# Kernel tuning notes

Hardware: AMD Instinct MI355X
Metric: run time of the kernel (lower is better)

Reference implementation:

```python
import jax, jax.numpy as jnp
import numpy as np

B, S, H, SSZ, IN = 1024, 100, 128, 100, 2


def _gru(x, h, Wih, Whh, bih, bhh):
    # PyTorch GRU cell: gates ordered (reset, update, new)
    gx = x @ Wih.T + bih
    gh = h @ Whh.T + bhh
    xr, xz, xn = jnp.split(gx, 3, axis=-1)
    hr, hz, hn = jnp.split(gh, 3, axis=-1)
    r = jax.nn.sigmoid(xr + hr)
    z = jax.nn.sigmoid(xz + hz)
    n = jnp.tanh(xn + r * hn)
    return (1.0 - z) * n + z * h


def _attn(inst_h, rnn_out, W, v):
    # inst_h: [B,S,H], rnn_out: [B,H] -> softmax attention weights [B,S]
    h = jnp.concatenate([inst_h, jnp.broadcast_to(rnn_out[:, None, :], inst_h.shape)], axis=-1)
    s = jax.nn.relu(jnp.einsum('bsk,kh->bsh', h, W)) @ v
    return jax.nn.softmax(s, axis=1)


def setup_inputs() -> dict:
    key = jax.random.key(0)
    k = jax.random.split(key, 32)
    p = lambda i, shape, sc=0.05: sc * jax.random.normal(k[i], shape, jnp.float32)
    instance = jax.random.uniform(k[0], (B, S, IN), jnp.float32)
    # solutions must be per-row permutations of node indices
    solution_1 = jnp.argsort(jax.random.uniform(k[1], (B, S)), axis=1).astype(jnp.int32)
    solution_2 = jnp.argsort(jax.random.uniform(k[2], (B, S)), axis=1).astype(jnp.int32)
    eps = jax.random.normal(k[3], (B, SSZ), jnp.float32)
    return dict(
        instance=instance, solution_1=solution_1, solution_2=solution_2, eps=eps,
        emb_i_W=p(4, (H, IN)), emb_i_b=jnp.zeros(H, jnp.float32),
        emb_r_W=p(5, (H, IN)), emb_r_b=jnp.zeros(H, jnp.float32),
        attn_W=p(6, (2 * H, H)), attn_v=p(7, (H,)),
        gru_Wih=p(8, (3 * H, H)), gru_Whh=p(9, (3 * H, H)),
        gru_bih=jnp.zeros(3 * H, jnp.float32), gru_bhh=jnp.zeros(3 * H, jnp.float32),
        grud_Wih=p(10, (3 * H, 2 * H)), grud_Whh=p(11, (3 * H, H)),
        grud_bih=jnp.zeros(3 * H, jnp.float32), grud_bhh=jnp.zeros(3 * H, jnp.float32),
        enc_fc1_W=p(12, (SSZ, H)), enc_fc1_b=jnp.zeros(SSZ, jnp.float32),
        enc_fc2_W=p(13, (SSZ, H)), enc_fc2_b=jnp.zeros(SSZ, jnp.float32),
        ptr_W=p(14, (2 * H, H)), ptr_v=p(15, (H,)),
        pfc1_W=p(16, (2 * H, 2 * H + SSZ)), pfc1_b=jnp.zeros(2 * H, jnp.float32),
        pfc2_W=p(17, (H, 2 * H)), pfc2_b=jnp.zeros(H, jnp.float32),
    )


def reference(instance, solution_1, solution_2, eps,
              emb_i_W, emb_i_b, emb_r_W, emb_r_b, attn_W, attn_v,
              gru_Wih, gru_Whh, gru_bih, gru_bhh,
              grud_Wih, grud_Whh, grud_bih, grud_bhh,
              enc_fc1_W, enc_fc1_b, enc_fc2_W, enc_fc2_b,
              ptr_W, ptr_v, pfc1_W, pfc1_b, pfc2_W, pfc2_b):
    b_idx = jnp.arange(B)
    inst_h = instance @ emb_i_W.T + emb_i_b  # [B,S,H]
    emb_r = lambda x: x @ emb_r_W.T + emb_r_b
    take = lambda ptr: instance[b_idx, ptr]  # gather node coords [B,IN]

    # ---------------- Encoder ----------------
    def enc_step(carry, ptr):
        h1, h2, ref_h = carry
        h1 = _gru(ref_h, h1, gru_Wih, gru_Whh, gru_bih, gru_bhh)
        a = _attn(inst_h, h1, attn_W, attn_v)
        context = jnp.einsum('bs,bsh->bh', a, inst_h)
        ref_h = emb_r(take(ptr))
        rnn_in = jnp.concatenate([ref_h, context], axis=-1)  # [B,2H]
        h2 = _gru(rnn_in, h2, grud_Wih, grud_Whh, grud_bih, grud_bhh)
        return (h1, h2, ref_h), None

    z0 = jnp.zeros((B, H), instance.dtype)
    ref_h0 = emb_r(take(solution_1[:, 0]))
    (_, h2, _), _ = jax.lax.scan(enc_step, (z0, z0, ref_h0), solution_1[:, 1:].T)
    mu = h2 @ enc_fc1_W.T + enc_fc1_b
    log_var = h2 @ enc_fc2_W.T + enc_fc2_b
    Z = mu + eps * jnp.exp(0.5 * log_var)

    # ---------------- Decoder (teacher forcing) ----------------
    mask0 = jnp.ones((B, S), instance.dtype).at[b_idx, solution_2[:, 0]].set(0.0)

    def dec_step(carry, ptr):
        h1, ref_in, mask = carry
        ref_h = emb_r(ref_in)
        h1 = _gru(ref_h, h1, gru_Wih, gru_Whh, gru_bih, gru_bhh)
        a = _attn(inst_h, h1, attn_W, attn_v)
        context = jnp.einsum('bs,bsh->bh', a, inst_h)
        fc_in = jnp.concatenate([context, Z, ref_h], axis=-1)  # [B, 2H+SSZ]
        fc_out = (fc_in @ pfc1_W.T + pfc1_b) @ pfc2_W.T + pfc2_b  # no activation, as in torch
        hcat = jnp.concatenate([inst_h, jnp.broadcast_to(fc_out[:, None, :], inst_h.shape)], axis=-1)
        logits = jnp.tanh(jnp.einsum('bsk,kh->bsh', hcat, ptr_W)) @ ptr_v  # [B,S]
        probs = jax.nn.softmax(logits + jnp.log(mask), axis=1)
        logp = jnp.log(probs[b_idx, ptr])
        pred = jnp.argmax(probs, axis=1)
        mask = mask.at[b_idx, ptr].set(0.0)  # tsp.update_mask: mark chosen node visited
        return (h1, take(ptr), mask), (pred, logp)

    init = (z0, take(solution_2[:, 0]), mask0)
    _, (preds, logps) = jax.lax.scan(dec_step, init, solution_2[:, 1:].T)
    tour_idx = jnp.concatenate([solution_2[:, :1], preds.T.astype(solution_2.dtype)], axis=1)
    tour_logp = logps.T  # [B, S-1]
    return (mu, log_var, Z, tour_idx, tour_logp)
```

## Files before the change

### kernel.cpp

```cpp
#include <hip/hip_runtime.h>
#include <math.h>

static constexpr int NB  = 1024;
static constexpr int NS  = 100;
static constexpr int NH  = 128;
static constexpr int GPB = 2;
static constexpr int NTHR = 256;
static constexpr int NBLK = NB / GPB;

static constexpr int OUT_MU = 0;
static constexpr int OUT_LV = NB * NS;
static constexpr int OUT_Z  = 2 * NB * NS;
static constexpr int OUT_TI = 3 * NB * NS;
static constexpr int OUT_LP = 4 * NB * NS;

#define NEGF (-3.4e38f)

template<int C4>
__device__ __forceinline__ void dot2x3f(const float* __restrict__ wr0,
        const float* __restrict__ wr1, const float* __restrict__ wr2,
        const float* __restrict__ x0, const float* __restrict__ x1,
        float& r00, float& r01, float& r10, float& r11, float& r20, float& r21)
{
    const float4* W0 = reinterpret_cast<const float4*>(wr0);
    const float4* W1 = reinterpret_cast<const float4*>(wr1);
    const float4* W2 = reinterpret_cast<const float4*>(wr2);
    const float4* X0 = reinterpret_cast<const float4*>(x0);
    const float4* X1 = reinterpret_cast<const float4*>(x1);
    float a00 = 0.f, a01 = 0.f, a10 = 0.f, a11 = 0.f, a20 = 0.f, a21 = 0.f;
    #pragma unroll 8
    for (int c = 0; c < C4; ++c) {
        float4 u0 = W0[c], u1 = W1[c], u2 = W2[c];
        float4 v0 = X0[c], v1 = X1[c];
        a00 = fmaf(u0.x, v0.x, a00); a00 = fmaf(u0.y, v0.y, a00); a00 = fmaf(u0.z, v0.z, a00); a00 = fmaf(u0.w, v0.w, a00);
        a01 = fmaf(u0.x, v1.x, a01); a01 = fmaf(u0.y, v1.y, a01); a01 = fmaf(u0.z, v1.z, a01); a01 = fmaf(u0.w, v1.w, a01);
        a10 = fmaf(u1.x, v0.x, a10); a10 = fmaf(u1.y, v0.y, a10); a10 = fmaf(u1.z, v0.z, a10); a10 = fmaf(u1.w, v0.w, a10);
        a11 = fmaf(u1.x, v1.x, a11); a11 = fmaf(u1.y, v1.y, a11); a11 = fmaf(u1.z, v1.z, a11); a11 = fmaf(u1.w, v1.w, a11);
        a20 = fmaf(u2.x, v0.x, a20); a20 = fmaf(u2.y, v0.y, a20); a20 = fmaf(u2.z, v0.z, a20); a20 = fmaf(u2.w, v0.w, a20);
        a21 = fmaf(u2.x, v1.x, a21); a21 = fmaf(u2.y, v1.y, a21); a21 = fmaf(u2.z, v1.z, a21); a21 = fmaf(u2.w, v1.w, a21);
    }
    r00 = a00; r01 = a01; r10 = a10; r11 = a11; r20 = a20; r21 = a21;
}

template<int C4>
__device__ __forceinline__ void dot2f(const float* __restrict__ w,
        const float* __restrict__ x0, const float* __restrict__ x1, float& r0, float& r1)
{
    const float4* W = reinterpret_cast<const float4*>(w);
    const float4* X0 = reinterpret_cast<const float4*>(x0);
    const float4* X1 = reinterpret_cast<const float4*>(x1);
    float a0 = 0.f, a1 = 0.f;
    #pragma unroll 8
    for (int c = 0; c < C4; ++c) {
        float4 u = W[c];
        float4 v0 = X0[c], v1 = X1[c];
        a0 = fmaf(u.x, v0.x, a0); a0 = fmaf(u.y, v0.y, a0); a0 = fmaf(u.z, v0.z, a0); a0 = fmaf(u.w, v0.w, a0);
        a1 = fmaf(u.x, v1.x, a1); a1 = fmaf(u.y, v1.y, a1); a1 = fmaf(u.z, v1.z, a1); a1 = fmaf(u.w, v1.w, a1);
    }
    r0 = a0; r1 = a1;
}

template<int C4>
__device__ __forceinline__ void dot1f(const float* __restrict__ w,
        const float* __restrict__ x0, float& r0)
{
    const float4* W = reinterpret_cast<const float4*>(w);
    const float4* X0 = reinterpret_cast<const float4*>(x0);
    float a0 = 0.f;
    #pragma unroll 8
    for (int c = 0; c < C4; ++c) {
        float4 u = W[c];
        float4 v0 = X0[c];
        a0 = fmaf(u.x, v0.x, a0); a0 = fmaf(u.y, v0.y, a0); a0 = fmaf(u.z, v0.z, a0); a0 = fmaf(u.w, v0.w, a0);
    }
    r0 = a0;
}

template<int C4>
__device__ __forceinline__ double dotwd(const float* __restrict__ w, const float* __restrict__ x)
{
    const float4* W = reinterpret_cast<const float4*>(w);
    double a = 0.0;
    #pragma unroll 8
    for (int c = 0; c < C4; ++c) {
        float4 u = W[c];
        const float* p = x + 4 * c;
        a = fma((double)u.x, (double)p[0], a);
        a = fma((double)u.y, (double)p[1], a);
        a = fma((double)u.z, (double)p[2], a);
        a = fma((double)u.w, (double)p[3], a);
    }
    return a;
}

__device__ __forceinline__ void gruc(const float* __restrict__ bih, const float* __restrict__ bhh,
        const float* __restrict__ pa, const float* __restrict__ pb, float* __restrict__ h, int j)
{
    double r = 1.0 / (1.0 + exp(-(((double)pa[j]        + (double)bih[j])        + ((double)pb[j]        + (double)bhh[j]))));
    double z = 1.0 / (1.0 + exp(-(((double)pa[NH + j]   + (double)bih[NH + j])   + ((double)pb[NH + j]   + (double)bhh[NH + j]))));
    double n = tanh(((double)pa[2*NH + j] + (double)bih[2*NH + j]) + r * ((double)pb[2*NH + j] + (double)bhh[2*NH + j]));
    h[j] = (float)((1.0 - z) * n + z * (double)h[j]);
}

__global__ __launch_bounds__(NTHR) void vae_v14(
    const float* __restrict__ instance, const int* __restrict__ sol1,
    const int* __restrict__ sol2, const float* __restrict__ eps,
    const float* __restrict__ emb_i_W, const float* __restrict__ emb_i_b,
    const float* __restrict__ emb_r_W, const float* __restrict__ emb_r_b,
    const float* __restrict__ attn_W, const float* __restrict__ attn_v,
    const float* __restrict__ gru_Wih, const float* __restrict__ gru_Whh,
    const float* __restrict__ gru_bih, const float* __restrict__ gru_bhh,
    const float* __restrict__ grud_Wih, const float* __restrict__ grud_Whh,
    const float* __restrict__ grud_bih, const float* __restrict__ grud_bhh,
    const float* __restrict__ efc1_W, const float* __restrict__ efc1_b,
    const float* __restrict__ efc2_W, const float* __restrict__ efc2_b,
    const float* __restrict__ ptr_W, const float* __restrict__ ptr_v,
    const float* __restrict__ pfc1_W, const float* __restrict__ pfc1_b,
    const float* __restrict__ pfc2_W, const float* __restrict__ pfc2_b,
    float* __restrict__ out)
{
    __shared__ float  s_x[GPB][360];
    __shared__ float  s_h1[GPB][NH], s_h2[GPB][NH], s_fco[GPB][NH];
    __shared__ float  s_fch[GPB][256];
    __shared__ float  s_pa[GPB][3 * NH], s_pb[GPB][3 * NH];
    __shared__ double s_qh[GPB][NH];
    __shared__ double s_qpA[GPB][NH], s_qpB[GPB][NH];
    __shared__ double2 dAa[NH], dAp[NH];
    __shared__ double dAba[NH], dAbp[NH];
    __shared__ float  s_lg[GPB][NS], s_a[GPB][NS];
    __shared__ float  s_c0[GPB][NS], s_c1[GPB][NS], s_msk[GPB][NS];
    __shared__ float  t_wi0[NH], t_wi1[NH], t_bi[NH];
    __shared__ float  t_wr0[NH], t_wr1[NH], t_br[NH];
    __shared__ float  t_va[NH], t_vp[NH];
    __shared__ float  t_gbih[3*NH], t_gbhh[3*NH], t_dbih[3*NH], t_dbhh[3*NH];
    __shared__ float  t_p1b[256], t_p2b[NH];
    __shared__ int    s_sol1[GPB][NS], s_sol2[GPB][NS];
    __shared__ float  s_red[GPB][2];
    __shared__ double s_redd[GPB][2];
    __shared__ int    s_ri[GPB][2];
    __shared__ float  s_rc0[GPB], s_rc1[GPB];

    const int tid = threadIdx.x;
    const int bbase = blockIdx.x * GPB;
    const int j = tid & (NH - 1);
    const int half = tid >> 7;
    const int g = half;
    const int lane = tid & 63;
    const int wid = (tid >> 6) & 1;

    if (tid < NH) {
        t_wi0[tid] = emb_i_W[2*tid]; t_wi1[tid] = emb_i_W[2*tid+1]; t_bi[tid] = emb_i_b[tid];
        t_wr0[tid] = emb_r_W[2*tid]; t_wr1[tid] = emb_r_W[2*tid+1]; t_br[tid] = emb_r_b[tid];
        t_va[tid] = attn_v[tid]; t_vp[tid] = ptr_v[tid];
        t_p2b[tid] = pfc2_b[tid];
    }
    t_p1b[tid] = pfc1_b[tid];
    for (int i = tid; i < 3 * NH; i += NTHR) {
        t_gbih[i] = gru_bih[i]; t_gbhh[i] = gru_bhh[i];
        t_dbih[i] = grud_bih[i]; t_dbhh[i] = grud_bhh[i];
    }
    for (int i = tid; i < GPB * NS; i += NTHR) {
        int gg = i / NS, s = i - gg * NS;
        s_c0[gg][s] = instance[(size_t)((bbase + gg) * NS + s) * 2 + 0];
        s_c1[gg][s] = instance[(size_t)((bbase + gg) * NS + s) * 2 + 1];
        s_sol1[gg][s] = sol1[(bbase + gg) * NS + s];
        s_sol2[gg][s] = sol2[(bbase + gg) * NS + s];
    }
    s_h1[g][j] = 0.f;
    s_h2[g][j] = 0.f;
    __syncthreads();
    {
        const float* Wm = (half == 0) ? attn_W : ptr_W;
        double a0 = 0.0, a1 = 0.0, ab = 0.0;
        for (int k = 0; k < NH; ++k) {
            double wv = (double)Wm[(size_t)k * NH + j];
            a0 = fma((double)t_wi0[k], wv, a0);
            a1 = fma((double)t_wi1[k], wv, a1);
            ab = fma((double)t_bi[k],  wv, ab);
        }
        if (half == 0) { dAa[j].x = a0; dAa[j].y = a1; dAba[j] = ab; }
        else           { dAp[j].x = a0; dAp[j].y = a1; dAbp[j] = ab; }
    }
    {
        int sp = s_sol1[g][0];
        s_x[g][j] = fmaf(s_c0[g][sp], t_wr0[j], fmaf(s_c1[g][sp], t_wr1[j], t_br[j]));
    }
    __syncthreads();

    for (int t = 1; t < NS; ++t) {
        if (half == 0) {
            float a00,a01,a10,a11,a20,a21;
            dot2x3f<32>(gru_Wih + (size_t)j * NH, gru_Wih + (size_t)(NH + j) * NH,
                        gru_Wih + (size_t)(2*NH + j) * NH, s_x[0], s_x[1],
                        a00,a01,a10,a11,a20,a21);
            s_pa[0][j] = a00;        s_pa[1][j] = a01;
            s_pa[0][NH + j] = a10;   s_pa[1][NH + j] = a11;
            s_pa[0][2*NH + j] = a20; s_pa[1][2*NH + j] = a21;
        } else {
            float a00,a01,a10,a11,a20,a21;
            dot2x3f<32>(gru_Whh + (size_t)j * NH, gru_Whh + (size_t)(NH + j) * NH,
                        gru_Whh + (size_t)(2*NH + j) * NH, s_h1[0], s_h1[1],
                        a00,a01,a10,a11,a20,a21);
            s_pb[0][j] = a00;        s_pb[1][j] = a01;
            s_pb[0][NH + j] = a10;   s_pb[1][NH + j] = a11;
            s_pb[0][2*NH + j] = a20; s_pb[1][2*NH + j] = a21;
        }
        __syncthreads();
        gruc(t_gbih, t_gbhh, s_pa[g], s_pb[g], s_h1[g], j);
        __syncthreads();
        {
            const float* col = attn_W + (size_t)NH * NH + j;
            const int k0 = half * 64;
            double a00=0.0,a01=0.0,a02=0.0,a03=0.0;
            double a10=0.0,a11=0.0,a12=0.0,a13=0.0;
            #pragma unroll 8
            for (int k = 0; k < 64; k += 4) {
                float w0 = col[(size_t)(k0+k+0) * NH];
                float w1 = col[(size_t)(k0+k+1) * NH];
                float w2 = col[(size_t)(k0+k+2) * NH];
                float w3 = col[(size_t)(k0+k+3) * NH];
                float4 h0 = *reinterpret_cast<const float4*>(&s_h1[0][k0+k]);
                float4 h1v = *reinterpret_cast<const float4*>(&s_h1[1][k0+k]);
                a00 = fma((double)w0, (double)h0.x, a00);
                a01 = fma((double)w1, (double)h0.y, a01);
                a02 = fma((double)w2, (double)h0.z, a02);
                a03 = fma((double)w3, (double)h0.w, a03);
                a10 = fma((double)w0, (double)h1v.x, a10);
                a11 = fma((double)w1, (double)h1v.y, a11);
                a12 = fma((double)w2, (double)h1v.z, a12);
                a13 = fma((double)w3, (double)h1v.w, a13);
            }
// ... 43 lines not shown
        }
        __syncthreads();
        {
            float w0 = t_wi0[j], w1 = t_wi1[j], bb = t_bi[j];
            double a0 = 0.0, a1 = 0.0, a2 = 0.0, a3 = 0.0;
            #pragma unroll 5
            for (int s = 0; s < NS; s += 4) {
                float ih0 = fmaf(s_c0[g][s+0], w0, fmaf(s_c1[g][s+0], w1, bb));
                float ih1 = fmaf(s_c0[g][s+1], w0, fmaf(s_c1[g][s+1], w1, bb));
                float ih2 = fmaf(s_c0[g][s+2], w0, fmaf(s_c1[g][s+2], w1, bb));
                float ih3 = fmaf(s_c0[g][s+3], w0, fmaf(s_c1[g][s+3], w1, bb));
                a0 += (double)s_a[g][s+0] * (double)ih0;
                a1 += (double)s_a[g][s+1] * (double)ih1;
                a2 += (double)s_a[g][s+2] * (double)ih2;
                a3 += (double)s_a[g][s+3] * (double)ih3;
            }
            s_x[g][NH + j] = (float)(((a0 + a1) + (a2 + a3)));
            int sp = s_sol1[g][t];
            s_x[g][j] = fmaf(s_c0[g][sp], t_wr0[j], fmaf(s_c1[g][sp], t_wr1[j], t_br[j]));
        }
        __syncthreads();
        if (half == 0) {
            float a00,a01,a10,a11,a20,a21;
            dot2x3f<64>(grud_Wih + (size_t)j * 256, grud_Wih + (size_t)(NH + j) * 256,
                        grud_Wih + (size_t)(2*NH + j) * 256, s_x[0], s_x[1],
                        a00,a01,a10,a11,a20,a21);
            s_pa[0][j] = a00;        s_pa[1][j] = a01;
            s_pa[0][NH + j] = a10;   s_pa[1][NH + j] = a11;
            s_pa[0][2*NH + j] = a20; s_pa[1][2*NH + j] = a21;
        } else {
            float a00,a01,a10,a11,a20,a21;
            dot2x3f<32>(grud_Whh + (size_t)j * NH, grud_Whh + (size_t)(NH + j) * NH,
                        grud_Whh + (size_t)(2*NH + j) * NH, s_h2[0], s_h2[1],
                        a00,a01,a10,a11,a20,a21);
            s_pb[0][j] = a00;        s_pb[1][j] = a01;
            s_pb[0][NH + j] = a10;   s_pb[1][NH + j] = a11;
            s_pb[0][2*NH + j] = a20; s_pb[1][2*NH + j] = a21;
        }
        __syncthreads();
        gruc(t_dbih, t_dbhh, s_pa[g], s_pb[g], s_h2[g], j);
        __syncthreads();
    }

    for (int idx = tid; idx < GPB * NS; idx += NTHR) {
        int gg = idx / NS, s = idx - gg * NS, b = bbase + gg;
        double mu = dotwd<32>(efc1_W + (size_t)s * NH, s_h2[gg]) + (double)efc1_b[s];
        double lv = dotwd<32>(efc2_W + (size_t)s * NH, s_h2[gg]) + (double)efc2_b[s];
        double z  = mu + (double)eps[(size_t)b * NS + s] * exp(0.5 * lv);
        out[OUT_MU + b * NS + s] = (float)mu;
        out[OUT_LV + b * NS + s] = (float)lv;
        out[OUT_Z  + b * NS + s] = (float)z;
        s_x[gg][NH + s] = (float)z;
    }
    for (int i = tid; i < GPB * NS; i += NTHR) {
        int gg = i / NS, s = i - gg * NS;
        s_msk[gg][s] = 1.f;
    }
    s_h1[g][j] = 0.f;
    __syncthreads();
    if (tid < GPB) {
        int b = bbase + tid;
        int s0 = s_sol2[tid][0];
        s_msk[tid][s0] = 0.f;
        s_rc0[tid] = s_c0[tid][s0];
        s_rc1[tid] = s_c1[tid][s0];
        out[OUT_TI + b * NS + 0] = (float)s0;
    }
    __syncthreads();

    for (int t = 1; t < NS; ++t) {
        s_x[g][228 + j] = fmaf(s_rc0[g], t_wr0[j], fmaf(s_rc1[g], t_wr1[j], t_br[j]));
        __syncthreads();
        if (half == 0) {
            float a00,a01,a10,a11,a20,a21;
            dot2x3f<32>(gru_Wih + (size_t)j * NH, gru_Wih + (size_t)(NH + j) * NH,
                        gru_Wih + (size_t)(2*NH + j) * NH, s_x[0]+228, s_x[1]+228,
                        a00,a01,a10,a11,a20,a21);
            s_pa[0][j] = a00;        s_pa[1][j] = a01;
            s_pa[0][NH + j] = a10;   s_pa[1][NH + j] = a11;
            s_pa[0][2*NH + j] = a20; s_pa[1][2*NH + j] = a21;
        } else {
            float a00,a01,a10,a11,a20,a21;
            dot2x3f<32>(gru_Whh + (size_t)j * NH, gru_Whh + (size_t)(NH + j) * NH,
                        gru_Whh + (size_t)(2*NH + j) * NH, s_h1[0], s_h1[1],
                        a00,a01,a10,a11,a20,a21);
            s_pb[0][j] = a00;        s_pb[1][j] = a01;
            s_pb[0][NH + j] = a10;   s_pb[1][NH + j] = a11;
            s_pb[0][2*NH + j] = a20; s_pb[1][2*NH + j] = a21;
        }
        __syncthreads();
        gruc(t_gbih, t_gbhh, s_pa[g], s_pb[g], s_h1[g], j);
        __syncthreads();
        {
            const float* col = attn_W + (size_t)NH * NH + j;
            const int k0 = half * 64;
            double a00=0.0,a01=0.0,a02=0.0,a03=0.0;
            double a10=0.0,a11=0.0,a12=0.0,a13=0.0;
            #pragma unroll 8
            for (int k = 0; k < 64; k += 4) {
                float w0 = col[(size_t)(k0+k+0) * NH];
                float w1 = col[(size_t)(k0+k+1) * NH];
                float w2 = col[(size_t)(k0+k+2) * NH];
                float w3 = col[(size_t)(k0+k+3) * NH];
                float4 h0 = *reinterpret_cast<const float4*>(&s_h1[0][k0+k]);
                float4 h1v = *reinterpret_cast<const float4*>(&s_h1[1][k0+k]);
                a00 = fma((double)w0, (double)h0.x, a00);
                a01 = fma((double)w1, (double)h0.y, a01);
                a02 = fma((double)w2, (double)h0.z, a02);
                a03 = fma((double)w3, (double)h0.w, a03);
                a10 = fma((double)w0, (double)h1v.x, a10);
                a11 = fma((double)w1, (double)h1v.y, a11);
                a12 = fma((double)w2, (double)h1v.z, a12);
                a13 = fma((double)w3, (double)h1v.w, a13);
            }
            if (half == 0) { s_qpA[0][j] = (a00+a01)+(a02+a03); s_qpA[1][j] = (a10+a11)+(a12+a13); }
            else           { s_qpB[0][j] = (a00+a01)+(a02+a03); s_qpB[1][j] = (a10+a11)+(a12+a13); }
        }
        __syncthreads();
        s_qh[g][j] = dAba[j] + (s_qpA[g][j] + s_qpB[g][j]);
        __syncthreads();
        if (j < NS) {
            double c00 = (double)s_c0[g][j], c10 = (double)s_c1[g][j];
            double acc0 = 0.0, acc1 = 0.0, acc2 = 0.0, acc3 = 0.0;
            #pragma unroll 4
            for (int h = 0; h < NH; h += 4) {
                double2 A0 = dAa[h+0], A1 = dAa[h+1], A2 = dAa[h+2], A3 = dAa[h+3];
                double p0 = fma(c00, A0.x, fma(c10, A0.y, s_qh[g][h+0]));
                double p1 = fma(c00, A1.x, fma(c10, A1.y, s_qh[g][h+1]));
                double p2 = fma(c00, A2.x, fma(c10, A2.y, s_qh[g][h+2]));
                double p3 = fma(c00, A3.x, fma(c10, A3.y, s_qh[g][h+3]));
                acc0 = fma(fmax(p0, 0.0), (double)t_va[h+0], acc0);
                acc1 = fma(fmax(p1, 0.0), (double)t_va[h+1], acc1);
                acc2 = fma(fmax(p2, 0.0), (double)t_va[h+2], acc2);
                acc3 = fma(fmax(p3, 0.0), (double)t_va[h+3], acc3);
            }
            s_lg[g][j] = (float)(((acc0 + acc1) + (acc2 + acc3)));
        }
        __syncthreads();
        {
            float a = s_lg[g][lane];
            float b = (lane + 64 < NS) ? s_lg[g][lane + 64] : NEGF;
            float m = fmaxf(a, b);
            m = fmaxf(m, __shfl_xor(m, 32)); m = fmaxf(m, __shfl_xor(m, 16));
            m = fmaxf(m, __shfl_xor(m, 8));  m = fmaxf(m, __shfl_xor(m, 4));
            m = fmaxf(m, __shfl_xor(m, 2));  m = fmaxf(m, __shfl_xor(m, 1));
            float fv = 0.f;
            if (j < NS) { fv = (float)exp((double)s_lg[g][j] - (double)m); s_a[g][j] = fv; }
            double ps = (double)fv;
            ps += __shfl_xor(ps, 32); ps += __shfl_xor(ps, 16);
            ps += __shfl_xor(ps, 8);  ps += __shfl_xor(ps, 4);
            ps += __shfl_xor(ps, 2);  ps += __shfl_xor(ps, 1);
            if (lane == 0) s_redd[g][wid] = ps;
        }
        __syncthreads();
        if (j < NS) {
            double se = s_redd[g][0] + s_redd[g][1];
            s_a[g][j] = (float)((double)s_a[g][j] / se);
        }
        __syncthreads();
        {
            float w0 = t_wi0[j], w1 = t_wi1[j], bb = t_bi[j];
            double a0 = 0.0, a1 = 0.0, a2 = 0.0, a3 = 0.0;
            #pragma unroll 5
            for (int s = 0; s < NS; s += 4) {
                float ih0 = fmaf(s_c0[g][s+0], w0, fmaf(s_c1[g][s+0], w1, bb));
                float ih1 = fmaf(s_c0[g][s+1], w0, fmaf(s_c1[g][s+1], w1, bb));
                float ih2 = fmaf(s_c0[g][s+2], w0, fmaf(s_c1[g][s+2], w1, bb));
                float ih3 = fmaf(s_c0[g][s+3], w0, fmaf(s_c1[g][s+3], w1, bb));
                a0 += (double)s_a[g][s+0] * (double)ih0;
                a1 += (double)s_a[g][s+1] * (double)ih1;
                a2 += (double)s_a[g][s+2] * (double)ih2;
                a3 += (double)s_a[g][s+3] * (double)ih3;
            }
            s_x[g][j] = (float)(((a0 + a1) + (a2 + a3)));
        }
        __syncthreads();
        {
            float r0, r1;
            dot2f<89>(pfc1_W + (size_t)tid * 356, s_x[0], s_x[1], r0, r1);
            float bb = t_p1b[tid];
            s_fch[0][tid] = r0 + bb; s_fch[1][tid] = r1 + bb;
        }
        __syncthreads();
        {
            float r0;
            dot1f<64>(pfc2_W + (size_t)j * 256, s_fch[g], r0);
            s_fco[g][j] = r0 + t_p2b[j];
        }
        __syncthreads();
        {
            const float* col = ptr_W + (size_t)NH * NH + j;
            const int k0 = half * 64;
            double a00=0.0,a01=0.0,a02=0.0,a03=0.0;
            double a10=0.0,a11=0.0,a12=0.0,a13=0.0;
            #pragma unroll 8
            for (int k = 0; k < 64; k += 4) {
                float w0 = col[(size_t)(k0+k+0) * NH];
                float w1 = col[(size_t)(k0+k+1) * NH];
                float w2 = col[(size_t)(k0+k+2) * NH];
                float w3 = col[(size_t)(k0+k+3) * NH];
                float4 f0 = *reinterpret_cast<const float4*>(&s_fco[0][k0+k]);
                float4 f1 = *reinterpret_cast<const float4*>(&s_fco[1][k0+k]);
                a00 = fma((double)w0, (double)f0.x, a00);
                a01 = fma((double)w1, (double)f0.y, a01);
                a02 = fma((double)w2, (double)f0.z, a02);
                a03 = fma((double)w3, (double)f0.w, a03);
                a10 = fma((double)w0, (double)f1.x, a10);
                a11 = fma((double)w1, (double)f1.y, a11);
                a12 = fma((double)w2, (double)f1.z, a12);
                a13 = fma((double)w3, (double)f1.w, a13);
            }
            if (half == 0) { s_qpA[0][j] = (a00+a01)+(a02+a03); s_qpA[1][j] = (a10+a11)+(a12+a13); }
            else           { s_qpB[0][j] = (a00+a01)+(a02+a03); s_qpB[1][j] = (a10+a11)+(a12+a13); }
        }
        __syncthreads();
        s_qh[g][j] = dAbp[j] + (s_qpA[g][j] + s_qpB[g][j]);
        __syncthreads();
        if (j < NS) {
            double c00 = (double)s_c0[g][j], c10 = (double)s_c1[g][j];
            double acc0 = 0.0, acc1 = 0.0, acc2 = 0.0, acc3 = 0.0;
            #pragma unroll 4
            for (int h = 0; h < NH; h += 4) {
                double2 A0 = dAp[h+0], A1 = dAp[h+1], A2 = dAp[h+2], A3 = dAp[h+3];
                double p0 = fma(c00, A0.x, fma(c10, A0.y, s_qh[g][h+0]));
                double p1 = fma(c00, A1.x, fma(c10, A1.y, s_qh[g][h+1]));
                double p2 = fma(c00, A2.x, fma(c10, A2.y, s_qh[g][h+2]));
                double p3 = fma(c00, A3.x, fma(c10, A3.y, s_qh[g][h+3]));
                acc0 = fma((double)tanhf((float)p0), (double)t_vp[h+0], acc0);
                acc1 = fma((double)tanhf((float)p1), (double)t_vp[h+1], acc1);
                acc2 = fma((double)tanhf((float)p2), (double)t_vp[h+2], acc2);
                acc3 = fma((double)tanhf((float)p3), (double)t_vp[h+3], acc3);
            }
            s_lg[g][j] = (float)(((acc0 + acc1) + (acc2 + acc3)));
        }
        __syncthreads();
        {
            float la = s_lg[g][lane];
            float ma = (s_msk[g][lane] > 0.f) ? la : NEGF;
            float lb = NEGF;
            if (lane + 64 < NS) lb = (s_msk[g][lane + 64] > 0.f) ? s_lg[g][lane + 64] : NEGF;
            float m = fmaxf(ma, lb);
            m = fmaxf(m, __shfl_xor(m, 32)); m = fmaxf(m, __shfl_xor(m, 16));
            m = fmaxf(m, __shfl_xor(m, 8));  m = fmaxf(m, __shfl_xor(m, 4));
            m = fmaxf(m, __shfl_xor(m, 2));  m = fmaxf(m, __shfl_xor(m, 1));
            float fv = 0.f;
            if (j < NS) {
                fv = (s_msk[g][j] > 0.f) ? (float)exp((double)s_lg[g][j] - (double)m) : 0.f;
                s_a[g][j] = fv;
            }
            float  bv = (j < NS) ? fv : -1.f;
            int    bi = (j < NS) ? j  : NS;
            double ps = (j < NS) ? (double)fv : 0.0;
            #pragma unroll
            for (int o = 32; o >= 1; o >>= 1) {
                float  ov = __shfl_xor(bv, o);
                int    oi = __shfl_xor(bi, o);
                double op = __shfl_xor(ps, o);
                ps += op;
                if (ov > bv || (ov == bv && oi < bi)) { bv = ov; bi = oi; }
            }
            if (lane == 0) { s_red[g][wid] = bv; s_ri[g][wid] = bi; s_redd[g][wid] = ps; }
        }
        __syncthreads();
        if (tid < GPB) {
            int gg = tid, b = bbase + gg;
            float m = -1.f; int mi = NS; double se = 0.0;
            for (int i = 0; i < 2; ++i) {
                se += s_redd[gg][i];
                float v = s_red[gg][i]; int vi = s_ri[gg][i];
                if (v > m || (v == m && vi < mi)) { m = v; mi = vi; }
            }
            int pt = s_sol2[gg][t];
            double logp = log((double)s_a[gg][pt] / se);
            out[OUT_TI + b * NS + t]             = (float)mi;
            out[OUT_LP + b * (NS - 1) + (t - 1)] = (float)logp;
            s_msk[gg][pt] = 0.f;
            s_rc0[gg] = s_c0[gg][pt];
            s_rc1[gg] = s_c1[gg][pt];
        }
        __syncthreads();
    }
}

extern "C" void kernel_launch(void* const* d_in, const int* in_sizes, int n_in,
                              void* d_out, int out_size, void* d_ws, size_t ws_size,
                              hipStream_t stream)
{
    (void)in_sizes; (void)n_in; (void)out_size; (void)d_ws; (void)ws_size;
    vae_v14<<<NBLK, NTHR, 0, stream>>>(
        (const float*)d_in[0], (const int*)d_in[1], (const int*)d_in[2], (const float*)d_in[3],
        (const float*)d_in[4], (const float*)d_in[5], (const float*)d_in[6], (const float*)d_in[7],
        (const float*)d_in[8], (const float*)d_in[9], (const float*)d_in[10], (const float*)d_in[11],
        (const float*)d_in[12], (const float*)d_in[13], (const float*)d_in[14], (const float*)d_in[15],
        (const float*)d_in[16], (const float*)d_in[17], (const float*)d_in[18], (const float*)d_in[19],
        (const float*)d_in[20], (const float*)d_in[21], (const float*)d_in[22], (const float*)d_in[23],
        (const float*)d_in[24], (const float*)d_in[25], (const float*)d_in[26], (const float*)d_in[27],
        (float*)d_out);
}
```

Measured before the change: 12.26 ms.

## Decouple GRU recurrence from per-step attention/pointer work, processing chunks of steps per wave

```diff
diff --git a/kernel.cpp b/kernel.cpp
--- a/kernel.cpp
+++ b/kernel.cpp
@@ -43,40 +43,6 @@
 }
 
 template<int C4>
-__device__ __forceinline__ void dot2f(const float* __restrict__ w,
-        const float* __restrict__ x0, const float* __restrict__ x1, float& r0, float& r1)
-{
-    const float4* W = reinterpret_cast<const float4*>(w);
-    const float4* X0 = reinterpret_cast<const float4*>(x0);
-    const float4* X1 = reinterpret_cast<const float4*>(x1);
-    float a0 = 0.f, a1 = 0.f;
-    #pragma unroll 8
-    for (int c = 0; c < C4; ++c) {
-        float4 u = W[c];
-        float4 v0 = X0[c], v1 = X1[c];
-        a0 = fmaf(u.x, v0.x, a0); a0 = fmaf(u.y, v0.y, a0); a0 = fmaf(u.z, v0.z, a0); a0 = fmaf(u.w, v0.w, a0);
-        a1 = fmaf(u.x, v1.x, a1); a1 = fmaf(u.y, v1.y, a1); a1 = fmaf(u.z, v1.z, a1); a1 = fmaf(u.w, v1.w, a1);
-    }
-    r0 = a0; r1 = a1;
-}
-
-template<int C4>
-__device__ __forceinline__ void dot1f(const float* __restrict__ w,
-        const float* __restrict__ x0, float& r0)
-{
-    const float4* W = reinterpret_cast<const float4*>(w);
-    const float4* X0 = reinterpret_cast<const float4*>(x0);
-    float a0 = 0.f;
-    #pragma unroll 8
-    for (int c = 0; c < C4; ++c) {
-        float4 u = W[c];
-        float4 v0 = X0[c];
-        a0 = fmaf(u.x, v0.x, a0); a0 = fmaf(u.y, v0.y, a0); a0 = fmaf(u.z, v0.z, a0); a0 = fmaf(u.w, v0.w, a0);
-    }
-    r0 = a0;
-}
-
-template<int C4>
 __device__ __forceinline__ double dotwd(const float* __restrict__ w, const float* __restrict__ x)
 {
     const float4* W = reinterpret_cast<const float4*>(w);
@@ -102,7 +68,7 @@
     h[j] = (float)((1.0 - z) * n + z * (double)h[j]);
 }
 
-__global__ __launch_bounds__(NTHR) void vae_v14(
+__global__ __launch_bounds__(NTHR) void vae_v15(
     const float* __restrict__ instance, const int* __restrict__ sol1,
     const int* __restrict__ sol2, const float* __restrict__ eps,
     const float* __restrict__ emb_i_W, const float* __restrict__ emb_i_b,
@@ -120,25 +86,33 @@
     float* __restrict__ out)
 {
     __shared__ float  s_x[GPB][360];
-    __shared__ float  s_h1[GPB][NH], s_h2[GPB][NH], s_fco[GPB][NH];
-    __shared__ float  s_fch[GPB][256];
+    __shared__ float  s_h1[GPB][NH], s_h2[GPB][NH];
     __shared__ float  s_pa[GPB][3 * NH], s_pb[GPB][3 * NH];
     __shared__ double s_qh[GPB][NH];
     __shared__ double s_qpA[GPB][NH], s_qpB[GPB][NH];
     __shared__ double2 dAa[NH], dAp[NH];
     __shared__ double dAba[NH], dAbp[NH];
     __shared__ float  s_lg[GPB][NS], s_a[GPB][NS];
-    __shared__ float  s_c0[GPB][NS], s_c1[GPB][NS], s_msk[GPB][NS];
+    __shared__ float  s_c0[GPB][NS], s_c1[GPB][NS];
     __shared__ float  t_wi0[NH], t_wi1[NH], t_bi[NH];
     __shared__ float  t_wr0[NH], t_wr1[NH], t_br[NH];
     __shared__ float  t_va[NH], t_vp[NH];
     __shared__ float  t_gbih[3*NH], t_gbhh[3*NH], t_dbih[3*NH], t_dbhh[3*NH];
     __shared__ float  t_p1b[256], t_p2b[NH];
     __shared__ int    s_sol1[GPB][NS], s_sol2[GPB][NS];
-    __shared__ float  s_red[GPB][2];
     __shared__ double s_redd[GPB][2];
-    __shared__ int    s_ri[GPB][2];
     __shared__ float  s_rc0[GPB], s_rc1[GPB];
+    __shared__ float    s_ref[GPB][NH];
+    __shared__ float    h1buf[8][GPB][NH];
+    __shared__ float    rcb0[GPB][9], rcb1[GPB][9];
+    __shared__ unsigned maskb[8][GPB][4];
+    __shared__ unsigned m_run[GPB][4];
+    __shared__ double   w_qh[4][NH];
+    __shared__ float    w_lg[4][NS];
+    __shared__ float    w_av[4][NS];
+    __shared__ float    w_x[4][360];
+    __shared__ float    w_fh[4][256];
+    __shared__ float    w_fo[4][NH];
 
     const int tid = threadIdx.x;
     const int bbase = blockIdx.x * GPB;
@@ -147,6 +121,7 @@
     const int g = half;
     const int lane = tid & 63;
     const int wid = (tid >> 6) & 1;
+    const int wv = tid >> 6;
 
     if (tid < NH) {
         t_wi0[tid] = emb_i_W[2*tid]; t_wi1[tid] = emb_i_W[2*tid+1]; t_bi[tid] = emb_i_b[tid];
@@ -173,10 +148,10 @@
         const float* Wm = (half == 0) ? attn_W : ptr_W;
         double a0 = 0.0, a1 = 0.0, ab = 0.0;
         for (int k = 0; k < NH; ++k) {
-            double wv = (double)Wm[(size_t)k * NH + j];
-            a0 = fma((double)t_wi0[k], wv, a0);
-            a1 = fma((double)t_wi1[k], wv, a1);
-            ab = fma((double)t_bi[k],  wv, ab);
+            double wv2 = (double)Wm[(size_t)k * NH + j];
+            a0 = fma((double)t_wi0[k], wv2, a0);
+            a1 = fma((double)t_wi1[k], wv2, a1);
+            ab = fma((double)t_bi[k],  wv2, ab);
         }
         if (half == 0) { dAa[j].x = a0; dAa[j].y = a1; dAba[j] = ab; }
         else           { dAp[j].x = a0; dAp[j].y = a1; dAbp[j] = ab; }
@@ -326,231 +301,257 @@
         out[OUT_Z  + b * NS + s] = (float)z;
         s_x[gg][NH + s] = (float)z;
     }
-    for (int i = tid; i < GPB * NS; i += NTHR) {
-        int gg = i / NS, s = i - gg * NS;
-        s_msk[gg][s] = 1.f;
-    }
     s_h1[g][j] = 0.f;
     __syncthreads();
     if (tid < GPB) {
         int b = bbase + tid;
         int s0 = s_sol2[tid][0];
-        s_msk[tid][s0] = 0.f;
+        m_run[tid][0] = 0xFFFFFFFFu; m_run[tid][1] = 0xFFFFFFFFu;
+        m_run[tid][2] = 0xFFFFFFFFu; m_run[tid][3] = 0xFu;
+        m_run[tid][s0 >> 5] &= ~(1u << (s0 & 31));
         s_rc0[tid] = s_c0[tid][s0];
         s_rc1[tid] = s_c1[tid][s0];
         out[OUT_TI + b * NS + 0] = (float)s0;
     }
     __syncthreads();
-
-    for (int t = 1; t < NS; ++t) {
-        s_x[g][228 + j] = fmaf(s_rc0[g], t_wr0[j], fmaf(s_rc1[g], t_wr1[j], t_br[j]));
-        __syncthreads();
-        if (half == 0) {
-            float a00,a01,a10,a11,a20,a21;
-            dot2x3f<32>(gru_Wih + (size_t)j * NH, gru_Wih + (size_t)(NH + j) * NH,
-                        gru_Wih + (size_t)(2*NH + j) * NH, s_x[0]+228, s_x[1]+228,
-                        a00,a01,a10,a11,a20,a21);
-            s_pa[0][j] = a00;        s_pa[1][j] = a01;
-            s_pa[0][NH + j] = a10;   s_pa[1][NH + j] = a11;
-            s_pa[0][2*NH + j] = a20; s_pa[1][2*NH + j] = a21;
-        } else {
-            float a00,a01,a10,a11,a20,a21;
-            dot2x3f<32>(gru_Whh + (size_t)j * NH, gru_Whh + (size_t)(NH + j) * NH,
-                        gru_Whh + (size_t)(2*NH + j) * NH, s_h1[0], s_h1[1],
-                        a00,a01,a10,a11,a20,a21);
-            s_pb[0][j] = a00;        s_pb[1][j] = a01;
-            s_pb[0][NH + j] = a10;   s_pb[1][NH + j] = a11;
-            s_pb[0][2*NH + j] = a20; s_pb[1][2*NH + j] = a21;
-        }
-        __syncthreads();
-        gruc(t_gbih, t_gbhh, s_pa[g], s_pb[g], s_h1[g], j);
-        __syncthreads();
-        {
-            const float* col = attn_W + (size_t)NH * NH + j;
-            const int k0 = half * 64;
-            double a00=0.0,a01=0.0,a02=0.0,a03=0.0;
-            double a10=0.0,a11=0.0,a12=0.0,a13=0.0;
-            #pragma unroll 8
-            for (int k = 0; k < 64; k += 4) {
-                float w0 = col[(size_t)(k0+k+0) * NH];
-                float w1 = col[(size_t)(k0+k+1) * NH];
-                float w2 = col[(size_t)(k0+k+2) * NH];
-                float w3 = col[(size_t)(k0+k+3) * NH];
-                float4 h0 = *reinterpret_cast<const float4*>(&s_h1[0][k0+k]);
-                float4 h1v = *reinterpret_cast<const float4*>(&s_h1[1][k0+k]);
-                a00 = fma((double)w0, (double)h0.x, a00);
-                a01 = fma((double)w1, (double)h0.y, a01);
-                a02 = fma((double)w2, (double)h0.z, a02);
-                a03 = fma((double)w3, (double)h0.w, a03);
-                a10 = fma((double)w0, (double)h1v.x, a10);
-                a11 = fma((double)w1, (double)h1v.y, a11);
-                a12 = fma((double)w2, (double)h1v.z, a12);
-                a13 = fma((double)w3, (double)h1v.w, a13);
-            }
-            if (half == 0) { s_qpA[0][j] = (a00+a01)+(a02+a03); s_qpA[1][j] = (a10+a11)+(a12+a13); }
-            else           { s_qpB[0][j] = (a00+a01)+(a02+a03); s_qpB[1][j] = (a10+a11)+(a12+a13); }
-        }
-        __syncthreads();
-        s_qh[g][j] = dAba[j] + (s_qpA[g][j] + s_qpB[g][j]);
-        __syncthreads();
-        if (j < NS) {
-            double c00 = (double)s_c0[g][j], c10 = (double)s_c1[g][j];
-            double acc0 = 0.0, acc1 = 0.0, acc2 = 0.0, acc3 = 0.0;
-            #pragma unroll 4
-            for (int h = 0; h < NH; h += 4) {
-                double2 A0 = dAa[h+0], A1 = dAa[h+1], A2 = dAa[h+2], A3 = dAa[h+3];
-                double p0 = fma(c00, A0.x, fma(c10, A0.y, s_qh[g][h+0]));
-                double p1 = fma(c00, A1.x, fma(c10, A1.y, s_qh[g][h+1]));
-                double p2 = fma(c00, A2.x, fma(c10, A2.y, s_qh[g][h+2]));
-                double p3 = fma(c00, A3.x, fma(c10, A3.y, s_qh[g][h+3]));
-                acc0 = fma(fmax(p0, 0.0), (double)t_va[h+0], acc0);
-                acc1 = fma(fmax(p1, 0.0), (double)t_va[h+1], acc1);
-                acc2 = fma(fmax(p2, 0.0), (double)t_va[h+2], acc2);
-                acc3 = fma(fmax(p3, 0.0), (double)t_va[h+3], acc3);
-            }
-            s_lg[g][j] = (float)(((acc0 + acc1) + (acc2 + acc3)));
-        }
-        __syncthreads();
-        {
-            float a = s_lg[g][lane];
-            float b = (lane + 64 < NS) ? s_lg[g][lane + 64] : NEGF;
-            float m = fmaxf(a, b);
-            m = fmaxf(m, __shfl_xor(m, 32)); m = fmaxf(m, __shfl_xor(m, 16));
-            m = fmaxf(m, __shfl_xor(m, 8));  m = fmaxf(m, __shfl_xor(m, 4));
-            m = fmaxf(m, __shfl_xor(m, 2));  m = fmaxf(m, __shfl_xor(m, 1));
-            float fv = 0.f;
-            if (j < NS) { fv = (float)exp((double)s_lg[g][j] - (double)m); s_a[g][j] = fv; }
-            double ps = (double)fv;
-            ps += __shfl_xor(ps, 32); ps += __shfl_xor(ps, 16);
-            ps += __shfl_xor(ps, 8);  ps += __shfl_xor(ps, 4);
-            ps += __shfl_xor(ps, 2);  ps += __shfl_xor(ps, 1);
-            if (lane == 0) s_redd[g][wid] = ps;
-        }
-        __syncthreads();
-        if (j < NS) {
-            double se = s_redd[g][0] + s_redd[g][1];
-            s_a[g][j] = (float)((double)s_a[g][j] / se);
-        }
-        __syncthreads();
-        {
-            float w0 = t_wi0[j], w1 = t_wi1[j], bb = t_bi[j];
-            double a0 = 0.0, a1 = 0.0, a2 = 0.0, a3 = 0.0;
-            #pragma unroll 5
-            for (int s = 0; s < NS; s += 4) {
-                float ih0 = fmaf(s_c0[g][s+0], w0, fmaf(s_c1[g][s+0], w1, bb));
-                float ih1 = fmaf(s_c0[g][s+1], w0, fmaf(s_c1[g][s+1], w1, bb));
-                float ih2 = fmaf(s_c0[g][s+2], w0, fmaf(s_c1[g][s+2], w1, bb));
-                float ih3 = fmaf(s_c0[g][s+3], w0, fmaf(s_c1[g][s+3], w1, bb));
-                a0 += (double)s_a[g][s+0] * (double)ih0;
-                a1 += (double)s_a[g][s+1] * (double)ih1;
-                a2 += (double)s_a[g][s+2] * (double)ih2;
-                a3 += (double)s_a[g][s+3] * (double)ih3;
-            }
-            s_x[g][j] = (float)(((a0 + a1) + (a2 + a3)));
-        }
-        __syncthreads();
-        {
-            float r0, r1;
-            dot2f<89>(pfc1_W + (size_t)tid * 356, s_x[0], s_x[1], r0, r1);
-            float bb = t_p1b[tid];
-            s_fch[0][tid] = r0 + bb; s_fch[1][tid] = r1 + bb;
-        }
-        __syncthreads();
-        {
-            float r0;
-            dot1f<64>(pfc2_W + (size_t)j * 256, s_fch[g], r0);
-            s_fco[g][j] = r0 + t_p2b[j];
-        }
-        __syncthreads();
-        {
-            const float* col = ptr_W + (size_t)NH * NH + j;
-            const int k0 = half * 64;
-            double a00=0.0,a01=0.0,a02=0.0,a03=0.0;
-            double a10=0.0,a11=0.0,a12=0.0,a13=0.0;
-            #pragma unroll 8
-            for (int k = 0; k < 64; k += 4) {
-                float w0 = col[(size_t)(k0+k+0) * NH];
-                float w1 = col[(size_t)(k0+k+1) * NH];
-                float w2 = col[(size_t)(k0+k+2) * NH];
-                float w3 = col[(size_t)(k0+k+3) * NH];
-                float4 f0 = *reinterpret_cast<const float4*>(&s_fco[0][k0+k]);
-                float4 f1 = *reinterpret_cast<const float4*>(&s_fco[1][k0+k]);
-                a00 = fma((double)w0, (double)f0.x, a00);
-                a01 = fma((double)w1, (double)f0.y, a01);
-                a02 = fma((double)w2, (double)f0.z, a02);
-                a03 = fma((double)w3, (double)f0.w, a03);
-                a10 = fma((double)w0, (double)f1.x, a10);
-                a11 = fma((double)w1, (double)f1.y, a11);
-                a12 = fma((double)w2, (double)f1.z, a12);
-                a13 = fma((double)w3, (double)f1.w, a13);
-            }
-            if (half == 0) { s_qpA[0][j] = (a00+a01)+(a02+a03); s_qpA[1][j] = (a10+a11)+(a12+a13); }
-            else           { s_qpB[0][j] = (a00+a01)+(a02+a03); s_qpB[1][j] = (a10+a11)+(a12+a13); }
-        }
-        __syncthreads();
-        s_qh[g][j] = dAbp[j] + (s_qpA[g][j] + s_qpB[g][j]);
-        __syncthreads();
-        if (j < NS) {
-            double c00 = (double)s_c0[g][j], c10 = (double)s_c1[g][j];
-            double acc0 = 0.0, acc1 = 0.0, acc2 = 0.0, acc3 = 0.0;
-            #pragma unroll 4
-            for (int h = 0; h < NH; h += 4) {
-                double2 A0 = dAp[h+0], A1 = dAp[h+1], A2 = dAp[h+2], A3 = dAp[h+3];
-                double p0 = fma(c00, A0.x, fma(c10, A0.y, s_qh[g][h+0]));
-                double p1 = fma(c00, A1.x, fma(c10, A1.y, s_qh[g][h+1]));
-                double p2 = fma(c00, A2.x, fma(c10, A2.y, s_qh[g][h+2]));
-                double p3 = fma(c00, A3.x, fma(c10, A3.y, s_qh[g][h+3]));
-                acc0 = fma((double)tanhf((float)p0), (double)t_vp[h+0], acc0);
-                acc1 = fma((double)tanhf((float)p1), (double)t_vp[h+1], acc1);
-                acc2 = fma((double)tanhf((float)p2), (double)t_vp[h+2], acc2);
-                acc3 = fma((double)tanhf((float)p3), (double)t_vp[h+3], acc3);
-            }
-            s_lg[g][j] = (float)(((acc0 + acc1) + (acc2 + acc3)));
-        }
-        __syncthreads();
-        {
-            float la = s_lg[g][lane];
-            float ma = (s_msk[g][lane] > 0.f) ? la : NEGF;
-            float lb = NEGF;
-            if (lane + 64 < NS) lb = (s_msk[g][lane + 64] > 0.f) ? s_lg[g][lane + 64] : NEGF;
-            float m = fmaxf(ma, lb);
-            m = fmaxf(m, __shfl_xor(m, 32)); m = fmaxf(m, __shfl_xor(m, 16));
-            m = fmaxf(m, __shfl_xor(m, 8));  m = fmaxf(m, __shfl_xor(m, 4));
-            m = fmaxf(m, __shfl_xor(m, 2));  m = fmaxf(m, __shfl_xor(m, 1));
-            float fv = 0.f;
-            if (j < NS) {
-                fv = (s_msk[g][j] > 0.f) ? (float)exp((double)s_lg[g][j] - (double)m) : 0.f;
-                s_a[g][j] = fv;
-            }
-            float  bv = (j < NS) ? fv : -1.f;
-            int    bi = (j < NS) ? j  : NS;
-            double ps = (j < NS) ? (double)fv : 0.0;
-            #pragma unroll
-            for (int o = 32; o >= 1; o >>= 1) {
-                float  ov = __shfl_xor(bv, o);
-                int    oi = __shfl_xor(bi, o);
-                double op = __shfl_xor(ps, o);
-                ps += op;
-                if (ov > bv || (ov == bv && oi < bi)) { bv = ov; bi = oi; }
-            }
-            if (lane == 0) { s_red[g][wid] = bv; s_ri[g][wid] = bi; s_redd[g][wid] = ps; }
-        }
-        __syncthreads();
+    s_ref[g][j] = fmaf(s_rc0[g], t_wr0[j], fmaf(s_rc1[g], t_wr1[j], t_br[j]));
+    __syncthreads();
+
+    for (int c = 0; c < 13; ++c) {
+        const int t0 = 1 + c * 8;
+        const int CHc = (t0 + 8 <= NS) ? 8 : (NS - t0);
         if (tid < GPB) {
-            int gg = tid, b = bbase + gg;
-            float m = -1.f; int mi = NS; double se = 0.0;
-            for (int i = 0; i < 2; ++i) {
-                se += s_redd[gg][i];
-                float v = s_red[gg][i]; int vi = s_ri[gg][i];
-                if (v > m || (v == m && vi < mi)) { m = v; mi = vi; }
-            }
-            int pt = s_sol2[gg][t];
-            double logp = log((double)s_a[gg][pt] / se);
-            out[OUT_TI + b * NS + t]             = (float)mi;
-            out[OUT_LP + b * (NS - 1) + (t - 1)] = (float)logp;
-            s_msk[gg][pt] = 0.f;
-            s_rc0[gg] = s_c0[gg][pt];
-            s_rc1[gg] = s_c1[gg][pt];
+            const int gg = tid;
+            for (int qi = 0; qi <= CHc; ++qi) {
+                int tt = t0 + qi;
+                if (qi < CHc) {
+                    maskb[qi][gg][0] = m_run[gg][0];
+                    maskb[qi][gg][1] = m_run[gg][1];
+                    maskb[qi][gg][2] = m_run[gg][2];
+                    maskb[qi][gg][3] = m_run[gg][3];
+                    int pt = s_sol2[gg][tt];
+                    m_run[gg][pt >> 5] &= ~(1u << (pt & 31));
+                }
+                int sp = s_sol2[gg][tt - 1];
+                rcb0[gg][qi] = s_c0[gg][sp];
+                rcb1[gg][qi] = s_c1[gg][sp];
+            }
+        }
+        __syncthreads();
+        for (int q = 0; q < CHc; ++q) {
+            if (half == 0) {
+                float a00,a01,a10,a11,a20,a21;
+                dot2x3f<32>(gru_Wih + (size_t)j * NH, gru_Wih + (size_t)(NH + j) * NH,
+                            gru_Wih + (size_t)(2*NH + j) * NH, s_ref[0], s_ref[1],
+                            a00,a01,a10,a11,a20,a21);
+                s_pa[0][j] = a00;        s_pa[1][j] = a01;
+                s_pa[0][NH + j] = a10;   s_pa[1][NH + j] = a11;
+                s_pa[0][2*NH + j] = a20; s_pa[1][2*NH + j] = a21;
+            } else {
+                float a00,a01,a10,a11,a20,a21;
+                dot2x3f<32>(gru_Whh + (size_t)j * NH, gru_Whh + (size_t)(NH + j) * NH,
+                            gru_Whh + (size_t)(2*NH + j) * NH, s_h1[0], s_h1[1],
+                            a00,a01,a10,a11,a20,a21);
+                s_pb[0][j] = a00;        s_pb[1][j] = a01;
+                s_pb[0][NH + j] = a10;   s_pb[1][NH + j] = a11;
+                s_pb[0][2*NH + j] = a20; s_pb[1][2*NH + j] = a21;
+            }
+            __syncthreads();
+            gruc(t_gbih, t_gbhh, s_pa[g], s_pb[g], s_h1[g], j);
+            h1buf[q][g][j] = s_h1[g][j];
+            s_ref[g][j] = fmaf(rcb0[g][q+1], t_wr0[j], fmaf(rcb1[g][q+1], t_wr1[j], t_br[j]));
+            __syncthreads();
+        }
+        for (int task = wv; task < 2 * CHc; task += 4) {
+            const int gg = task & 1;
+            const int qq = task >> 1;
+            const int tt = t0 + qq;
+            double* qh = w_qh[wv];
+            float*  lg = w_lg[wv];
+            float*  av = w_av[wv];
+            float*  xx = w_x[wv];
+            float*  fh = w_fh[wv];
+            float*  fo = w_fo[wv];
+            const float* h1t = &h1buf[qq][gg][0];
+            #pragma unroll
+            for (int p = 0; p < 2; ++p) {
+                const int jj = lane + (p << 6);
+                const float* col = attn_W + (size_t)NH * NH + jj;
+                double a0=0.0,a1=0.0,a2=0.0,a3=0.0;
+                #pragma unroll 8
+                for (int k = 0; k < NH; k += 4) {
+                    a0 = fma((double)col[(size_t)(k+0)*NH], (double)h1t[k+0], a0);
+                    a1 = fma((double)col[(size_t)(k+1)*NH], (double)h1t[k+1], a1);
+                    a2 = fma((double)col[(size_t)(k+2)*NH], (double)h1t[k+2], a2);
+                    a3 = fma((double)col[(size_t)(k+3)*NH], (double)h1t[k+3], a3);
+                }
+                qh[jj] = dAba[jj] + ((a0+a1)+(a2+a3));
+            }
+            #pragma unroll
+            for (int p = 0; p < 2; ++p) {
+                const int jj = lane + (p << 6);
+                if (jj < NS) {
+                    double c00 = (double)s_c0[gg][jj], c10 = (double)s_c1[gg][jj];
+                    double acc0=0.0,acc1=0.0,acc2=0.0,acc3=0.0;
+                    #pragma unroll 4
+                    for (int h = 0; h < NH; h += 4) {
+                        double2 A0=dAa[h+0],A1=dAa[h+1],A2=dAa[h+2],A3=dAa[h+3];
+                        double p0 = fma(c00,A0.x,fma(c10,A0.y,qh[h+0]));
+                        double p1 = fma(c00,A1.x,fma(c10,A1.y,qh[h+1]));
+                        double p2 = fma(c00,A2.x,fma(c10,A2.y,qh[h+2]));
+                        double p3 = fma(c00,A3.x,fma(c10,A3.y,qh[h+3]));
+                        acc0 = fma(fmax(p0,0.0),(double)t_va[h+0],acc0);
+                        acc1 = fma(fmax(p1,0.0),(double)t_va[h+1],acc1);
+                        acc2 = fma(fmax(p2,0.0),(double)t_va[h+2],acc2);
+                        acc3 = fma(fmax(p3,0.0),(double)t_va[h+3],acc3);
+                    }
+                    lg[jj] = (float)((acc0+acc1)+(acc2+acc3));
+                }
+            }
+            {
+                float v1 = lg[lane];
+                float v2 = (lane + 64 < NS) ? lg[lane + 64] : NEGF;
+                float m = fmaxf(v1, v2);
+                m = fmaxf(m, __shfl_xor(m,32)); m = fmaxf(m, __shfl_xor(m,16));
+                m = fmaxf(m, __shfl_xor(m,8));  m = fmaxf(m, __shfl_xor(m,4));
+                m = fmaxf(m, __shfl_xor(m,2));  m = fmaxf(m, __shfl_xor(m,1));
+                float f1 = (float)exp((double)v1 - (double)m);
+                float f2 = 0.f;
+                if (lane + 64 < NS) f2 = (float)exp((double)v2 - (double)m);
+                double ps = (double)f1 + (double)f2;
+                ps += __shfl_xor(ps,32); ps += __shfl_xor(ps,16); ps += __shfl_xor(ps,8);
+                ps += __shfl_xor(ps,4);  ps += __shfl_xor(ps,2);  ps += __shfl_xor(ps,1);
+                av[lane] = (float)((double)f1 / ps);
+                if (lane + 64 < NS) av[lane + 64] = (float)((double)f2 / ps);
+            }
+            #pragma unroll
+            for (int p = 0; p < 2; ++p) {
+                const int jj = lane + (p << 6);
+                float w0 = t_wi0[jj], w1 = t_wi1[jj], bb2 = t_bi[jj];
+                double a0=0.0,a1=0.0,a2=0.0,a3=0.0;
+                #pragma unroll 5
+                for (int s = 0; s < NS; s += 4) {
+                    float ih0 = fmaf(s_c0[gg][s+0], w0, fmaf(s_c1[gg][s+0], w1, bb2));
+                    float ih1 = fmaf(s_c0[gg][s+1], w0, fmaf(s_c1[gg][s+1], w1, bb2));
+                    float ih2 = fmaf(s_c0[gg][s+2], w0, fmaf(s_c1[gg][s+2], w1, bb2));
+                    float ih3 = fmaf(s_c0[gg][s+3], w0, fmaf(s_c1[gg][s+3], w1, bb2));
+                    a0 += (double)av[s+0] * (double)ih0;
+                    a1 += (double)av[s+1] * (double)ih1;
+                    a2 += (double)av[s+2] * (double)ih2;
+                    a3 += (double)av[s+3] * (double)ih3;
+                }
+                xx[jj] = (float)((a0+a1)+(a2+a3));
+            }
+            {
+                xx[NH + lane] = s_x[gg][NH + lane];
+                if (lane + 64 < NS) xx[NH + lane + 64] = s_x[gg][NH + lane + 64];
+                float rc0v = rcb0[gg][qq], rc1v = rcb1[gg][qq];
+                xx[228 + lane]      = fmaf(rc0v, t_wr0[lane],      fmaf(rc1v, t_wr1[lane],      t_br[lane]));
+                xx[228 + lane + 64] = fmaf(rc0v, t_wr0[lane + 64], fmaf(rc1v, t_wr1[lane + 64], t_br[lane + 64]));
+            }
+            #pragma unroll
+            for (int p = 0; p < 4; ++p) {
+                const int i = lane + (p << 6);
+                const float4* W = reinterpret_cast<const float4*>(pfc1_W + (size_t)i * 356);
+                float a0 = 0.f;
+                #pragma unroll 8
+                for (int c4 = 0; c4 < 89; ++c4) {
+                    float4 u = W[c4];
+                    const int k = 4 * c4;
+                    a0 = fmaf(u.x, xx[k+0], a0); a0 = fmaf(u.y, xx[k+1], a0);
+                    a0 = fmaf(u.z, xx[k+2], a0); a0 = fmaf(u.w, xx[k+3], a0);
+                }
+                fh[i] = a0 + t_p1b[i];
+            }
+            #pragma unroll
+            for (int p = 0; p < 2; ++p) {
+                const int jj = lane + (p << 6);
+                const float4* W = reinterpret_cast<const float4*>(pfc2_W + (size_t)jj * 256);
+                float a0 = 0.f;
+                #pragma unroll 8
+                for (int c4 = 0; c4 < 64; ++c4) {
+                    float4 u = W[c4];
+                    const int k = 4 * c4;
+                    a0 = fmaf(u.x, fh[k+0], a0); a0 = fmaf(u.y, fh[k+1], a0);
+                    a0 = fmaf(u.z, fh[k+2], a0); a0 = fmaf(u.w, fh[k+3], a0);
+                }
+                fo[jj] = a0 + t_p2b[jj];
+            }
+            #pragma unroll
+            for (int p = 0; p < 2; ++p) {
+                const int jj = lane + (p << 6);
+                const float* col = ptr_W + (size_t)NH * NH + jj;
+                double a0=0.0,a1=0.0,a2=0.0,a3=0.0;
+                #pragma unroll 8
+                for (int k = 0; k < NH; k += 4) {
+                    a0 = fma((double)col[(size_t)(k+0)*NH], (double)fo[k+0], a0);
+                    a1 = fma((double)col[(size_t)(k+1)*NH], (double)fo[k+1], a1);
+                    a2 = fma((double)col[(size_t)(k+2)*NH], (double)fo[k+2], a2);
+                    a3 = fma((double)col[(size_t)(k+3)*NH], (double)fo[k+3], a3);
+                }
+                qh[jj] = dAbp[jj] + ((a0+a1)+(a2+a3));
+            }
+            #pragma unroll
+            for (int p = 0; p < 2; ++p) {
+                const int jj = lane + (p << 6);
+                if (jj < NS) {
+                    double c00 = (double)s_c0[gg][jj], c10 = (double)s_c1[gg][jj];
+                    double acc0=0.0,acc1=0.0,acc2=0.0,acc3=0.0;
+                    #pragma unroll 4
+                    for (int h = 0; h < NH; h += 4) {
+                        double2 A0=dAp[h+0],A1=dAp[h+1],A2=dAp[h+2],A3=dAp[h+3];
+                        double p0 = fma(c00,A0.x,fma(c10,A0.y,qh[h+0]));
+                        double p1 = fma(c00,A1.x,fma(c10,A1.y,qh[h+1]));
+                        double p2 = fma(c00,A2.x,fma(c10,A2.y,qh[h+2]));
+                        double p3 = fma(c00,A3.x,fma(c10,A3.y,qh[h+3]));
+                        acc0 = fma((double)tanhf((float)p0),(double)t_vp[h+0],acc0);
+                        acc1 = fma((double)tanhf((float)p1),(double)t_vp[h+1],acc1);
+                        acc2 = fma((double)tanhf((float)p2),(double)t_vp[h+2],acc2);
+                        acc3 = fma((double)tanhf((float)p3),(double)t_vp[h+3],acc3);
+                    }
+                    lg[jj] = (float)((acc0+acc1)+(acc2+acc3));
+                }
+            }
+            {
+                const unsigned* mwp = &maskb[qq][gg][0];
+                bool u1 = (mwp[lane >> 5] >> (lane & 31)) & 1u;
+                float l1 = lg[lane];
+                float c1v = u1 ? l1 : NEGF;
+                bool u2 = false; float l2 = 0.f, c2v = NEGF;
+                if (lane + 64 < NS) {
+                    u2 = (mwp[(lane + 64) >> 5] >> (lane & 31)) & 1u;
+                    l2 = lg[lane + 64];
+                    c2v = u2 ? l2 : NEGF;
+                }
+                float m = fmaxf(c1v, c2v);
+                m = fmaxf(m, __shfl_xor(m,32)); m = fmaxf(m, __shfl_xor(m,16));
+                m = fmaxf(m, __shfl_xor(m,8));  m = fmaxf(m, __shfl_xor(m,4));
+                m = fmaxf(m, __shfl_xor(m,2));  m = fmaxf(m, __shfl_xor(m,1));
+                float f1 = u1 ? (float)exp((double)l1 - (double)m) : 0.f;
+                av[lane] = f1;
+                float f2 = 0.f;
+                if (lane + 64 < NS) {
+                    f2 = u2 ? (float)exp((double)l2 - (double)m) : 0.f;
+                    av[lane + 64] = f2;
+                }
+                float bv = f1; int bi = lane;
+                if (lane + 64 < NS && f2 > bv) { bv = f2; bi = lane + 64; }
+                double ps = (double)f1 + (double)f2;
+                #pragma unroll
+                for (int o = 32; o >= 1; o >>= 1) {
+                    float  ov = __shfl_xor(bv, o);
+                    int    oi = __shfl_xor(bi, o);
+                    double op = __shfl_xor(ps, o);
+                    ps += op;
+                    if (ov > bv || (ov == bv && oi < bi)) { bv = ov; bi = oi; }
+                }
+                if (lane == 0) {
+                    int pt = s_sol2[gg][tt];
+                    double logp = log((double)av[pt] / ps);
+                    out[OUT_TI + (size_t)(bbase + gg) * NS + tt]            = (float)bi;
+                    out[OUT_LP + (size_t)(bbase + gg) * (NS - 1) + (tt - 1)] = (float)logp;
+                }
+            }
         }
         __syncthreads();
     }
@@ -561,7 +562,7 @@
                               hipStream_t stream)
 {
     (void)in_sizes; (void)n_in; (void)out_size; (void)d_ws; (void)ws_size;
-    vae_v14<<<NBLK, NTHR, 0, stream>>>(
+    vae_v15<<<NBLK, NTHR, 0, stream>>>(
         (const float*)d_in[0], (const int*)d_in[1], (const int*)d_in[2], (const float*)d_in[3],
         (const float*)d_in[4], (const float*)d_in[5], (const float*)d_in[6], (const float*)d_in[7],
         (const float*)d_in[8], (const float*)d_in[9], (const float*)d_in[10], (const float*)d_in[11],
```

Result: slower. 14.80 ms (+20.7%).
